# Performance work log

Hardware: AMD Instinct MI355X
Metric: run time of the kernel (lower is better)

Reference implementation:

```python
import jax, jax.numpy as jnp
import numpy as np

N, E = 100000, 800000
D_IN, D_H, D_EMB = 64, 64, 64
L, S = 2, 4
NOISE_SCALE, MIN_U = 0.1, 1e-6


def _xavier(k, shape):
    lim = float(np.sqrt(6.0 / (shape[0] + shape[1])))
    return jax.random.uniform(k, shape, jnp.float32, -lim, lim)


def setup_inputs():
    key = jax.random.key(0)
    ks = jax.random.split(key, 7)
    x = jax.random.normal(ks[0], (N, D_IN), jnp.float32)
    edge_index = jax.random.randint(ks[1], (2, E), 0, N)
    parent_mask = jax.random.bernoulli(ks[2], 0.7, (E,))
    Wi = _xavier(ks[3], (D_IN, D_H))
    bi = jnp.zeros((D_H,), jnp.float32)
    msg_W = jnp.stack([_xavier(jax.random.fold_in(ks[4], l), (2 * D_H, D_H)) for l in range(L)])
    msg_b = jnp.zeros((L, D_H), jnp.float32)
    upd_W = jnp.stack([_xavier(jax.random.fold_in(ks[5], l), (2 * D_H, D_H)) for l in range(L)])
    upd_b = jnp.zeros((L, D_H), jnp.float32)
    Wf = _xavier(ks[6], (D_H, D_EMB))
    bf = jnp.zeros((D_EMB,), jnp.float32)
    return dict(x=x, edge_index=edge_index, parent_mask=parent_mask, Wi=Wi, bi=bi,
                msg_W=msg_W, msg_b=msg_b, upd_W=upd_W, upd_b=upd_b, Wf=Wf, bf=bf)


def _gnn(x, src, dst, mask_f, cnt_inv, Wi, bi, msg_W, msg_b, upd_W, upd_b, Wf, bf):
    # input_proj -> relu, then L rounds of (gather -> message linear -> masked
    # scatter-mean -> update linear -> relu), then final_proj.
    h = jax.nn.relu(x @ Wi + bi)
    for l in range(L):
        Wm, Wu = msg_W[l], upd_W[l]
        # message = Linear(concat(x_i, x_j)); x_i = h[dst] (target), x_j = h[src] (source)
        msg = h[dst] @ Wm[:D_H] + h[src] @ Wm[D_H:] + msg_b[l]  # [E, D_H]
        agg = jax.ops.segment_sum(msg * mask_f[:, None], dst, num_segments=N) * cnt_inv[:, None]
        # update = Linear(concat(x, aggr_out))
        h = jax.nn.relu(h @ Wu[:D_H] + agg @ Wu[D_H:] + upd_b[l])
    return h @ Wf + bf  # [N, D_EMB]


def reference(x, edge_index, parent_mask, Wi, bi, msg_W, msg_b, upd_W, upd_b, Wf, bf):
    src, dst = edge_index[0], edge_index[1]
    mask_f = parent_mask.astype(x.dtype)
    # scatter-mean over causal-parent edges only (0 for nodes without parents, as in PyG)
    cnt = jax.ops.segment_sum(mask_f, dst, num_segments=N)
    cnt_inv = 1.0 / jnp.maximum(cnt, 1.0)
    params = (Wi, bi, msg_W, msg_b, upd_W, upd_b, Wf, bf)
    causal_z = _gnn(x, src, dst, mask_f, cnt_inv, *params)
    # Monte Carlo uncertainty: S perturbed causal embeddings, trace of sample covariance
    noise = jax.random.normal(jax.random.key(42), (S, N, D_IN), x.dtype) * NOISE_SCALE
    zs = jax.lax.map(lambda n: _gnn(x + n, src, dst, mask_f, cnt_inv, *params), noise)  # [S, N, D_EMB]
    mean = zs.mean(axis=0)
    u = jnp.sum((zs - mean[None]) ** 2, axis=(0, 2)) / (S - 1)
    u = jnp.maximum(u, MIN_U)
    return causal_z, u
```

## Files before the change

kernel.cpp:

```cpp
#include <hip/hip_runtime.h>
#include <stdint.h>

#define NN 100000
#define EE 800000
#define GEMM_BX 1563
#define WSTR 72
#define SLAB ((size_t)NN * 64)
#define EDGE_CAP 2304

#define MA_TOTAL 6379
#define MB_TOTAL 7814

typedef unsigned short u16;
typedef __attribute__((ext_vector_type(8))) short bf16x8;
typedef __attribute__((ext_vector_type(4))) float f32x4;

__device__ __forceinline__ uint32_t f2bf(float f) {
  uint32_t u = __float_as_uint(f);
  return (u + 0x7fffu + ((u >> 16) & 1u)) >> 16;
}

__device__ __forceinline__ void tf_round(uint32_t& x0, uint32_t& x1, int r) {
  x0 += x1;
  x1 = (x1 << r) | (x1 >> (32 - r));
  x1 ^= x0;
}

__device__ __forceinline__ void threefry_0_42(uint32_t c0, uint32_t c1,
                                              uint32_t& o0, uint32_t& o1) {
  const uint32_t ks0 = 0u, ks1 = 42u, ks2 = 0x1BD11BDAu ^ 42u;
  uint32_t x0 = c0 + ks0, x1 = c1 + ks1;
  tf_round(x0, x1, 13); tf_round(x0, x1, 15); tf_round(x0, x1, 26); tf_round(x0, x1, 6);
  x0 += ks1; x1 += ks2 + 1u;
  tf_round(x0, x1, 17); tf_round(x0, x1, 29); tf_round(x0, x1, 16); tf_round(x0, x1, 24);
  x0 += ks2; x1 += ks0 + 2u;
  tf_round(x0, x1, 13); tf_round(x0, x1, 15); tf_round(x0, x1, 26); tf_round(x0, x1, 6);
  x0 += ks0; x1 += ks1 + 3u;
  tf_round(x0, x1, 17); tf_round(x0, x1, 29); tf_round(x0, x1, 16); tf_round(x0, x1, 24);
  x0 += ks1; x1 += ks2 + 4u;
  tf_round(x0, x1, 13); tf_round(x0, x1, 15); tf_round(x0, x1, 26); tf_round(x0, x1, 6);
  x0 += ks2; x1 += ks0 + 5u;
  o0 = x0; o1 = x1;
}

__device__ __forceinline__ float noise_val(int s, int n, int d) {
  uint32_t f = (uint32_t)s * 6400000u + (uint32_t)n * 64u + (uint32_t)d;
  uint32_t o0, o1;
  threefry_0_42(0u, f, o0, o1);
  uint32_t bits = o0 ^ o1;
  float v = __uint_as_float((bits >> 9) | 0x3f800000u) - 1.0f;
  const float LO = -0.99999994f;
  float u = v * 2.0f + LO;
  u = fmaxf(u, LO);
  float w = -__logf(fmaf(-u, u, 1.0f));
  float ww = w - 2.5f;
  float p = 2.81022636e-08f;
  p = fmaf(p, ww, 3.43273939e-07f);
  p = fmaf(p, ww, -3.5233877e-06f);
  p = fmaf(p, ww, -4.39150654e-06f);
  p = fmaf(p, ww, 0.00021858087f);
  p = fmaf(p, ww, -0.00125372503f);
  p = fmaf(p, ww, -0.00417768164f);
  p = fmaf(p, ww, 0.246640727f);
  p = fmaf(p, ww, 1.50140941f);
  if (__any(w >= 5.0f)) {
    float ws = sqrtf(w) - 3.0f;
    float p2 = -0.000200214257f;
    p2 = fmaf(p2, ws, 0.000100950558f);
    p2 = fmaf(p2, ws, 0.00134934322f);
    p2 = fmaf(p2, ws, -0.00367342844f);
    p2 = fmaf(p2, ws, 0.00573950773f);
    p2 = fmaf(p2, ws, -0.0076224613f);
    p2 = fmaf(p2, ws, 0.00943887047f);
    p2 = fmaf(p2, ws, 1.00167406f);
    p2 = fmaf(p2, ws, 2.83297682f);
    p = (w < 5.0f) ? p : p2;
  }
  return 0.141421356f * (p * u);
}

__device__ __forceinline__ int mask_at(const void* m, int e, int mode) {
  if (mode == 0) return ((const int*)m)[e] != 0;
  if (mode == 1) return ((const unsigned char*)m)[e] != 0;
  return ((const float*)m)[e] != 0.0f;
}

__global__ void k_pre(const unsigned* mw, int* mode_out,
                      const float* Wi, const float* Wf,
                      const float* msg_b, const float* upd_W,
                      u16* WiT, u16* WfT, float* C1) {
  int b = blockIdx.x, t = threadIdx.x;
  if (b == 0) {
    __shared__ int nonbin, nonfloat;
    if (t == 0) { nonbin = 0; nonfloat = 0; }
    __syncthreads();
    int lb = 0, lf = 0;
    for (int i = t; i < 4096; i += 256) {
      unsigned v = mw[i];
      if (v > 1u) lb = 1;
      if (v != 0u && v != 0x3F800000u) lf = 1;
    }
    if (lb) atomicOr(&nonbin, 1);
    if (lf) atomicOr(&nonfloat, 1);
    __syncthreads();
    if (t == 0)
      mode_out[0] = (nonbin == 0) ? 0 : ((nonfloat == 0) ? 2 : 1);
    return;
  }
  if (b <= 2) {
    const float* W = (b == 1) ? Wi : Wf;
    u16* WT = (b == 1) ? WiT : WfT;
    for (int o = t; o < 4096; o += 256) {
      int k = o >> 6, n = o & 63;
      WT[n * 64 + k] = (u16)f2bf(W[k * 64 + n]);
    }
    return;
  }
  int l = b - 3;
  const float* Wu2 = upd_W + l * 8192 + 4096;
  if (t < 64) {
    float acc = 0.f;
    for (int j = 0; j < 64; ++j) acc = fmaf(msg_b[l * 64 + j], Wu2[j * 64 + t], acc);
    C1[l * 64 + t] = acc;
  }
}

__global__ void k_scan_a(const int* cnt, int* blockSums) {
  __shared__ int sd[256];
  int t = threadIdx.x;
  int base = blockIdx.x * 1024 + t * 4;
  int s = 0;
  #pragma unroll
  for (int j = 0; j < 4; ++j) {
    int i = base + j;
    if (i < NN) s += cnt[i];
  }
  sd[t] = s;
  __syncthreads();
  for (int off = 128; off > 0; off >>= 1) {
    if (t < off) sd[t] += sd[t + off];
    __syncthreads();
  }
  if (t == 0) blockSums[blockIdx.x] = sd[0];
}

__global__ void k_scan_b(int* blockSums, int nb, int* total_out) {
  __shared__ int sd[128];
  int t = threadIdx.x;
  int v = (t < nb) ? blockSums[t] : 0;
  sd[t] = v;
  __syncthreads();
  for (int off = 1; off < 128; off <<= 1) {
    int x = (t >= off) ? sd[t - off] : 0;
    __syncthreads();
    sd[t] += x;
    __syncthreads();
  }
  if (t < nb) blockSums[t] = sd[t] - v;
  if (t == 0) total_out[0] = sd[127];
}

__global__ void k_scan_c(const int* cnt, const int* blockOffs, int* row_ptr,
                         int* cursor, float* cinv) {
  __shared__ int sd[256];
  int t = threadIdx.x;
  int base = blockIdx.x * 1024 + t * 4;
  int v[4], s = 0;
  #pragma unroll
  for (int j = 0; j < 4; ++j) {
    int i = base + j;
    v[j] = (i < NN) ? cnt[i] : 0;
    s += v[j];
  }
  sd[t] = s;
  __syncthreads();
  for (int off = 1; off < 256; off <<= 1) {
    int x = (t >= off) ? sd[t - off] : 0;
    __syncthreads();
    sd[t] += x;
    __syncthreads();
  }
  int excl = sd[t] - s + blockOffs[blockIdx.x];
  #pragma unroll
  for (int j = 0; j < 4; ++j) {
    int i = base + j;
    if (i < NN) {
      row_ptr[i] = excl;
      cursor[i] = excl;
      cinv[i] = 1.0f / fmaxf((float)v[j], 1.0f);
    }
    excl += v[j];
  }
}

__device__ __forceinline__ void mm4(const u16* lW, int m16, int q,
                                    bf16x8 a0, bf16x8 a1, f32x4 (&acc)[4]) {
  #pragma unroll
  for (int nt = 0; nt < 4; ++nt) {
    const u16* wp = lW + (nt * 16 + m16) * WSTR + q * 8;
    bf16x8 b0 = *(const bf16x8*)(wp);
    bf16x8 b1 = *(const bf16x8*)(wp + 32);
    acc[nt] = __builtin_amdgcn_mfma_f32_16x16x32_bf16(a0, b0, acc[nt], 0, 0, 0);
    acc[nt] = __builtin_amdgcn_mfma_f32_16x16x32_bf16(a1, b1, acc[nt], 0, 0, 0);
  }
}

__device__ __forceinline__ void stage_W(const u16* __restrict__ WT, u16* lW) {
  int t = threadIdx.x;
  int r = t >> 2, seg = (t & 3) * 16;
  const uint4* p = (const uint4*)(WT + r * 64 + seg);
  uint4 a = p[0], b = p[1];
  *(uint4*)(lW + r * WSTR + seg) = a;
  *(uint4*)(lW + r * WSTR + seg + 8) = b;
}

__device__ __forceinline__ void stage_H(const u16* __restrict__ Hin, int R0, u16* lT) {
  int t = threadIdx.x;
  int r = t >> 2, seg = (t & 3) * 16;
  int gr = R0 + r;
  uint4 a = {0, 0, 0, 0}, b = {0, 0, 0, 0};
  if (gr < NN) {
    const uint4* p = (const uint4*)(Hin + (size_t)gr * 64 + seg);
    a = p[0]; b = p[1];
  }
  *(uint4*)(lT + r * WSTR + seg) = a;
  *(uint4*)(lT + r * WSTR + seg + 8) = b;
}

__device__ __forceinline__ void input_block(int tile, int inst,
                                            const float* __restrict__ x,
                                            const u16* __restrict__ WiT,
                                            const float* __restrict__ bi,
                                            u16* __restrict__ HoutB,
                                            u16* lW, float* lB) {
  int t = threadIdx.x;
  stage_W(WiT, lW);
  if (t < 64) lB[t] = bi[t];
  int R0 = tile * 64;
  int l = t & 63, w = t >> 6;
  int m16 = l & 15, q = l >> 4;
  int arow = w * 16 + m16;
  int gra = R0 + arow;
  float v[16];
  if (gra < NN) {
    const float4* p0 = (const float4*)(x + (size_t)gra * 64 + q * 8);
    const float4* p1 = (const float4*)(x + (size_t)gra * 64 + q * 8 + 32);
    float4 a = p0[0], b = p0[1], c = p1[0], d = p1[1];
    v[0] = a.x;  v[1] = a.y;  v[2] = a.z;  v[3] = a.w;
    v[4] = b.x;  v[5] = b.y;  v[6] = b.z;  v[7] = b.w;
    v[8] = c.x;  v[9] = c.y;  v[10] = c.z; v[11] = c.w;
    v[12] = d.x; v[13] = d.y; v[14] = d.z; v[15] = d.w;
    if (inst > 0) {
      int s = inst - 1;
      #pragma unroll
      for (int j = 0; j < 8; ++j) v[j] += noise_val(s, gra, q * 8 + j);
      #pragma unroll
      for (int j = 0; j < 8; ++j) v[8 + j] += noise_val(s, gra, q * 8 + 32 + j);
    }
  } else {
    #pragma unroll
    for (int j = 0; j < 16; ++j) v[j] = 0.f;
  }
  union UB { uint32_t u[4]; bf16x8 vv; };
  UB ua, ub;
  #pragma unroll
  for (int jj = 0; jj < 4; ++jj) {
    ua.u[jj] = f2bf(v[2 * jj]) | (f2bf(v[2 * jj + 1]) << 16);
    ub.u[jj] = f2bf(v[8 + 2 * jj]) | (f2bf(v[8 + 2 * jj + 1]) << 16);
  }
  __syncthreads();
  f32x4 acc[4] = {{0.f, 0.f, 0.f, 0.f}, {0.f, 0.f, 0.f, 0.f},
                  {0.f, 0.f, 0.f, 0.f}, {0.f, 0.f, 0.f, 0.f}};
  mm4(lW, m16, q, ua.vv, ub.vv, acc);
  u16* Hout = HoutB + (size_t)inst * SLAB;
  #pragma unroll
  for (int nt = 0; nt < 4; ++nt) {
    int c = nt * 16 + m16;
    #pragma unroll
    for (int r_ = 0; r_ < 4; ++r_) {
      int row = w * 16 + q * 4 + r_;
      int gr = R0 + row;
      if (gr < NN) {
        float z = fmaxf(acc[nt][r_] + lB[c], 0.f);
        Hout[(size_t)gr * 64 + c] = (u16)f2bf(z);
      }
    }
  }
}

__global__ __launch_bounds__(256) void k_megaA(
    const void* __restrict__ mask, const int* __restrict__ dst,
    int* __restrict__ cnt, const int* __restrict__ mode_p,
    const float* __restrict__ x, const u16* __restrict__ WiT,
    const float* __restrict__ bi, u16* __restrict__ HoutB,
    const float* __restrict__ msg_W, const float* __restrict__ upd_W,
    u16* __restrict__ Wu1T, u16* __restrict__ A1T, u16* __restrict__ A2T) {
  __shared__ __align__(16) u16 lW[64 * WSTR];
  __shared__ float lB[64];
  int t = threadIdx.x;
  int bid = blockIdx.x;

  if (bid < 6250) {
    if ((bid & 1) == 0) {
      int e = (bid >> 1) * 256 + t;
      if (e < EE && mask_at(mask, e, *mode_p)) atomicAdd(&cnt[dst[e]], 1);
      return;
    }
    int idx = bid >> 1;
    input_block(idx % GEMM_BX, idx / GEMM_BX, x, WiT, bi, HoutB, lW, lB);
    return;
  }
  if (bid == 6250) {
    input_block(3125 % GEMM_BX, 3125 / GEMM_BX, x, WiT, bi, HoutB, lW, lB);
    return;
  }
  int blk = bid - 6251;
  int l = blk >> 6, b = blk & 63;
  const float* WmT = msg_W + l * 8192;
  const float* WmB = WmT + 4096;
  const float* Wu1 = upd_W + l * 8192;
  const float* Wu2 = Wu1 + 4096;
  float* sd1 = (float*)lW;
  float* sd2 = sd1 + 256;
  int a = t & 63, part = t >> 6;
  float a1 = 0.f, a2 = 0.f;
  #pragma unroll
  for (int jj = 0; jj < 16; ++jj) {
    int j = part * 16 + jj;
    float w2 = Wu2[j * 64 + b];
    a1 = fmaf(WmT[a * 64 + j], w2, a1);
    a2 = fmaf(WmB[a * 64 + j], w2, a2);
  }
  sd1[part * 64 + a] = a1;
  sd2[part * 64 + a] = a2;
  __syncthreads();
  if (t < 64) {
    float s1 = sd1[t] + sd1[64 + t] + sd1[128 + t] + sd1[192 + t];
    float s2 = sd2[t] + sd2[64 + t] + sd2[128 + t] + sd2[192 + t];
    int o = l * 4096 + b * 64 + t;
    A1T[o] = (u16)f2bf(s1);
    A2T[o] = (u16)f2bf(s2);
    Wu1T[o] = (u16)f2bf(Wu1[t * 64 + b]);
  }
}

__global__ __launch_bounds__(256) void k_megaB(
    const void* __restrict__ mask, const int* __restrict__ src,
    const int* __restrict__ dst, int* __restrict__ cursor,
    int* __restrict__ col, const int* __restrict__ mode_p,
    const float* __restrict__ x, const u16* __restrict__ WiT,
    const float* __restrict__ bi, u16* __restrict__ HoutB) {
  __shared__ __align__(16) u16 lW[64 * WSTR];
  __shared__ float lB[64];
  int t = threadIdx.x;
  int bid = blockIdx.x;

  int idx;
  if (bid < 6250) {
    if ((bid & 1) == 0) {
      int e = (bid >> 1) * 256 + t;
      if (e < EE && mask_at(mask, e, *mode_p)) {
        int p = atomicAdd(&cursor[dst[e]], 1);
        col[p] = src[e];
      }
      return;
    }
    idx = bid >> 1;
  } else {
    idx = 3125 + (bid - 6250);
  }
  input_block(idx % GEMM_BX, 2 + idx / GEMM_BX, x, WiT, bi, HoutB, lW, lB);
}

__global__ __launch_bounds__(256) void k_layer(const u16* __restrict__ HinB,
                                               u16* __restrict__ HoutB,
                                               const int* __restrict__ row_ptr,
                                               const int* __restrict__ col,
                                               const float* __restrict__ cinv,
                                               const u16* __restrict__ Wu1T,
                                               const u16* __restrict__ A1T,
                                               const u16* __restrict__ A2T,
                                               const float* __restrict__ b0,
                                               const float* __restrict__ c1) {
  __shared__ __align__(16) u16 lS0[64 * WSTR];
  __shared__ __align__(16) u16 lS1[64 * WSTR];
  __shared__ __align__(16) u16 lW[64 * WSTR];
  __shared__ float lB[128];
  __shared__ float lG[64];
  __shared__ int   lRP[65];
  int* lEdge = (int*)lW;

  int t = threadIdx.x;
  int R0 = blockIdx.x * 64;
  int instBase = blockIdx.y * 2;
  bool two = (instBase + 1) < 5;
  const u16* Hin0 = HinB + (size_t)instBase * SLAB;
  const u16* Hin1 = Hin0 + (two ? SLAB : 0);
  u16* Hout0 = HoutB + (size_t)instBase * SLAB;
  u16* Hout1 = Hout0 + SLAB;

  if (t < 65) {
    int idx = R0 + t;
    if (idx > NN) idx = NN;
    lRP[t] = row_ptr[idx];
  }
  if (t < 64) {
    lB[t] = b0[t];
    lB[64 + t] = c1[t];
  }
  __syncthreads();

  int e0 = lRP[0];
  int nE = lRP[64] - e0;
  bool inLds = (nE <= EDGE_CAP);
  if (inLds) {
    for (int i = t; i < nE; i += 256) lEdge[i] = col[e0 + i];
  }
  if (t < 64) lG[t] = (lRP[t + 1] > lRP[t]) ? 1.f : 0.f;
  __syncthreads();

  {
    int sub = t >> 3, lane8 = t & 7;
    int f0 = lane8 * 8;
    const u16* hb0 = Hin0 + f0;
    const u16* hb1 = Hin1 + f0;
    #pragma unroll
    for (int bb = 0; bb < 2; ++bb) {
      int r = bb * 32 + sub;
      int n = R0 + r;
      float g[8], h[8];
      #pragma unroll
      for (int j = 0; j < 8; ++j) { g[j] = 0.f; h[j] = 0.f; }
      if (n < NN) {
        int e = lRP[r], end = lRP[r + 1];
        int last = end - 1;
        for (; e < end; e += 4) {
          int idx4[4];
          #pragma unroll
          for (int j = 0; j < 4; ++j) {
            int ee = e + j;
            ee = (ee < last) ? ee : last;
            idx4[j] = inLds ? lEdge[ee - e0] : col[ee];
          }
          uint4 P[4];
          #pragma unroll
          for (int j = 0; j < 4; ++j)
            P[j] = *(const uint4*)(hb0 + ((unsigned)idx4[j] << 6));
          uint4 Q[4];
          if (two) {
            #pragma unroll
            for (int j = 0; j < 4; ++j)
              Q[j] = *(const uint4*)(hb1 + ((unsigned)idx4[j] << 6));
          }
          #pragma unroll
          for (int j = 1; j < 4; ++j) {
            bool ok = (e + j) < end;
            P[j].x = ok ? P[j].x : 0u;
            P[j].y = ok ? P[j].y : 0u;
            P[j].z = ok ? P[j].z : 0u;
            P[j].w = ok ? P[j].w : 0u;
            if (two) {
              Q[j].x = ok ? Q[j].x : 0u;
              Q[j].y = ok ? Q[j].y : 0u;
              Q[j].z = ok ? Q[j].z : 0u;
              Q[j].w = ok ? Q[j].w : 0u;
            }
          }
          #pragma unroll
          for (int j = 0; j < 4; ++j) {
            uint4 v = P[j];
            g[0] += __uint_as_float(v.x << 16);
            g[1] += __uint_as_float(v.x & 0xffff0000u);
            g[2] += __uint_as_float(v.y << 16);
            g[3] += __uint_as_float(v.y & 0xffff0000u);
            g[4] += __uint_as_float(v.z << 16);
            g[5] += __uint_as_float(v.z & 0xffff0000u);
            g[6] += __uint_as_float(v.w << 16);
            g[7] += __uint_as_float(v.w & 0xffff0000u);
          }
          if (two) {
            #pragma unroll
            for (int j = 0; j < 4; ++j) {
              uint4 v = Q[j];
              h[0] += __uint_as_float(v.x << 16);
              h[1] += __uint_as_float(v.x & 0xffff0000u);
              h[2] += __uint_as_float(v.y << 16);
              h[3] += __uint_as_float(v.y & 0xffff0000u);
              h[4] += __uint_as_float(v.z << 16);
              h[5] += __uint_as_float(v.z & 0xffff0000u);
              h[6] += __uint_as_float(v.w << 16);
              h[7] += __uint_as_float(v.w & 0xffff0000u);
            }
          }
        }
        float ci = cinv[n];
        #pragma unroll
        for (int j = 0; j < 8; ++j) { g[j] *= ci; h[j] *= ci; }
      }
      uint4 pk;
      pk.x = f2bf(g[0]) | (f2bf(g[1]) << 16);
      pk.y = f2bf(g[2]) | (f2bf(g[3]) << 16);
      pk.z = f2bf(g[4]) | (f2bf(g[5]) << 16);
      pk.w = f2bf(g[6]) | (f2bf(g[7]) << 16);
      *(uint4*)(lS0 + r * WSTR + f0) = pk;
      if (two) {
        uint4 pk2;
        pk2.x = f2bf(h[0]) | (f2bf(h[1]) << 16);
        pk2.y = f2bf(h[2]) | (f2bf(h[3]) << 16);
        pk2.z = f2bf(h[4]) | (f2bf(h[5]) << 16);
        pk2.w = f2bf(h[6]) | (f2bf(h[7]) << 16);
        *(uint4*)(lS1 + r * WSTR + f0) = pk2;
      }
    }
  }
  __syncthreads();

  int l = t & 63, w = t >> 6;
  int m16 = l & 15, q = l >> 4;
  int arow = w * 16 + m16;
  int gra = R0 + arow;
  bf16x8 zz = {0, 0, 0, 0, 0, 0, 0, 0};
  bf16x8 fa0_0 = zz, fa1_0 = zz, fa0_1 = zz, fa1_1 = zz;
  if (gra < NN) {
    const u16* ap = Hin0 + (size_t)gra * 64 + q * 8;
    fa0_0 = *(const bf16x8*)(ap);
    fa1_0 = *(const bf16x8*)(ap + 32);
    if (two) {
      const u16* ap1 = Hin1 + (size_t)gra * 64 + q * 8;
      fa0_1 = *(const bf16x8*)(ap1);
      fa1_1 = *(const bf16x8*)(ap1 + 32);
    }
  }

  stage_W(Wu1T, lW);
  __syncthreads();

  float gA = lG[arow];
  f32x4 acc0[4] = {{0.f, 0.f, 0.f, 0.f}, {0.f, 0.f, 0.f, 0.f},
                   {0.f, 0.f, 0.f, 0.f}, {0.f, 0.f, 0.f, 0.f}};
  f32x4 acc1[4] = {{0.f, 0.f, 0.f, 0.f}, {0.f, 0.f, 0.f, 0.f},
                   {0.f, 0.f, 0.f, 0.f}, {0.f, 0.f, 0.f, 0.f}};
  mm4(lW, m16, q, fa0_0, fa1_0, acc0);
  if (two) mm4(lW, m16, q, fa0_1, fa1_1, acc1);
  __syncthreads();
  stage_W(A1T, lW);
  __syncthreads();
  {
    bf16x8 ga0 = (gA != 0.f) ? fa0_0 : zz;
    bf16x8 ga1 = (gA != 0.f) ? fa1_0 : zz;
    mm4(lW, m16, q, ga0, ga1, acc0);
    if (two) {
      bf16x8 gb0 = (gA != 0.f) ? fa0_1 : zz;
      bf16x8 gb1 = (gA != 0.f) ? fa1_1 : zz;
      mm4(lW, m16, q, gb0, gb1, acc1);
    }
  }
  __syncthreads();
  stage_W(A2T, lW);
  __syncthreads();
  {
    const u16* sRow = lS0 + arow * WSTR + q * 8;
    bf16x8 fs0 = *(const bf16x8*)(sRow);
    bf16x8 fs1 = *(const bf16x8*)(sRow + 32);
    mm4(lW, m16, q, fs0, fs1, acc0);
    if (two) {
      const u16* sRow1 = lS1 + arow * WSTR + q * 8;
      bf16x8 ft0 = *(const bf16x8*)(sRow1);
      bf16x8 ft1 = *(const bf16x8*)(sRow1 + 32);
      mm4(lW, m16, q, ft0, ft1, acc1);
    }
  }
  #pragma unroll
  for (int nt = 0; nt < 4; ++nt) {
    int c = nt * 16 + m16;
    #pragma unroll
    for (int r_ = 0; r_ < 4; ++r_) {
      int row = w * 16 + q * 4 + r_;
      int gr = R0 + row;
      if (gr < NN) {
        float bias = lB[c] + lG[row] * lB[64 + c];
        float v0 = fmaxf(acc0[nt][r_] + bias, 0.f);
        Hout0[(size_t)gr * 64 + c] = (u16)f2bf(v0);
        if (two) {
          float v1 = fmaxf(acc1[nt][r_] + bias, 0.f);
          Hout1[(size_t)gr * 64 + c] = (u16)f2bf(v1);
        }
      }
    }
  }
}

__global__ __launch_bounds__(256) void k_final(const u16* __restrict__ HinB,
                                               const u16* __restrict__ WfT,
                                               const float* __restrict__ bfv,
                                               float* __restrict__ outCausal,
                                               float* __restrict__ out_u) {
  __shared__ __align__(16) u16 lT[64 * WSTR];
  __shared__ __align__(16) u16 lW[64 * WSTR];
  __shared__ float lB[64];
  int t = threadIdx.x;
  int R0 = blockIdx.x * 64;
  stage_W(WfT, lW);
  if (t < 64) lB[t] = bfv[t];
  int l = t & 63, w = t >> 6;
  int m16 = l & 15, q = l >> 4;
  float s1[16], s2[16];
  #pragma unroll
  for (int j = 0; j < 16; ++j) { s1[j] = 0.f; s2[j] = 0.f; }

  for (int inst = 0; inst < 5; ++inst) {
    __syncthreads();
    stage_H(HinB + (size_t)inst * SLAB, R0, lT);
    __syncthreads();
    const u16* aRow = lT + (w * 16 + m16) * WSTR + q * 8;
    bf16x8 fa0 = *(const bf16x8*)(aRow);
    bf16x8 fa1 = *(const bf16x8*)(aRow + 32);
    f32x4 acc[4] = {{0.f, 0.f, 0.f, 0.f}, {0.f, 0.f, 0.f, 0.f},
                    {0.f, 0.f, 0.f, 0.f}, {0.f, 0.f, 0.f, 0.f}};
    mm4(lW, m16, q, fa0, fa1, acc);
    #pragma unroll
    for (int nt = 0; nt < 4; ++nt) {
      int c = nt * 16 + m16;
      #pragma unroll
      for (int r_ = 0; r_ < 4; ++r_) {
        float z = acc[nt][r_] + lB[c];
        if (inst == 0) {
          int gr = R0 + w * 16 + q * 4 + r_;
          if (gr < NN) outCausal[(size_t)gr * 64 + c] = z;
        } else {
          s1[nt * 4 + r_] += z;
          s2[nt * 4 + r_] = fmaf(z, z, s2[nt * 4 + r_]);
        }
      }
    }
  }
  #pragma unroll
  for (int r_ = 0; r_ < 4; ++r_) {
    float pr = 0.f;
    #pragma unroll
    for (int nt = 0; nt < 4; ++nt) {
      float a = s1[nt * 4 + r_];
      pr += s2[nt * 4 + r_] - 0.25f * a * a;
    }
    #pragma unroll
    for (int msk = 1; msk < 16; msk <<= 1)
      pr += __shfl_xor(pr, msk, 64);
    if (m16 == 0) {
      int gr = R0 + w * 16 + q * 4 + r_;
      if (gr < NN) out_u[gr] = fmaxf(pr * (1.0f / 3.0f), 1e-6f);
    }
  }
}

extern "C" void kernel_launch(void* const* d_in, const int* in_sizes, int n_in,
                              void* d_out, int out_size, void* d_ws, size_t ws_size,
                              hipStream_t stream) {
  const float* x      = (const float*)d_in[0];
  const int*   eidx   = (const int*)d_in[1];
  const void*  mask   = d_in[2];
  const float* Wi     = (const float*)d_in[3];
  const float* bi     = (const float*)d_in[4];
  const float* msg_W  = (const float*)d_in[5];
  const float* msg_b  = (const float*)d_in[6];
  const float* upd_W  = (const float*)d_in[7];
  const float* upd_b  = (const float*)d_in[8];
  const float* Wf     = (const float*)d_in[9];
  const float* bfv    = (const float*)d_in[10];

  const int* src = eidx;
  const int* dst = eidx + EE;

  char* ws = (char*)d_ws;
  size_t off = 0;
  auto alloc = [&](size_t bytes) -> void* {
    void* p = ws + off;
    off += (bytes + 255) & ~(size_t)255;
    return p;
  };

  int*   cnt     = (int*)alloc(NN * sizeof(int));
  float* cinv    = (float*)alloc(NN * sizeof(float));
  int*   row_ptr = (int*)alloc((NN + 1) * sizeof(int));
  int*   cursor  = (int*)alloc(NN * sizeof(int));
  int*   col     = (int*)alloc(EE * sizeof(int));
  int*   bsums   = (int*)alloc(128 * sizeof(int));
  int*   mode_p  = (int*)alloc(sizeof(int));
  u16*   Wu1T    = (u16*)alloc(2 * 4096 * sizeof(u16));
  u16*   A1T     = (u16*)alloc(2 * 4096 * sizeof(u16));
  u16*   A2T     = (u16*)alloc(2 * 4096 * sizeof(u16));
  u16*   WiT     = (u16*)alloc(4096 * sizeof(u16));
  u16*   WfT     = (u16*)alloc(4096 * sizeof(u16));
  float* C1      = (float*)alloc(2 * 64 * sizeof(float));
  u16*   HA      = (u16*)alloc(5 * SLAB * sizeof(u16));
  u16*   HB      = (u16*)alloc(5 * SLAB * sizeof(u16));

  float* out_causal = (float*)d_out;
  float* out_u      = (float*)d_out + SLAB;

  k_pre<<<5, 256, 0, stream>>>((const unsigned*)mask, mode_p, Wi, Wf,
                               msg_b, upd_W, WiT, WfT, C1);
  hipMemsetAsync(cnt, 0, NN * sizeof(int), stream);

  k_megaA<<<MA_TOTAL, 256, 0, stream>>>(mask, dst, cnt, mode_p,
                                        x, WiT, bi, HA,
                                        msg_W, upd_W, Wu1T, A1T, A2T);

  const int SCAN_BLKS = (NN + 1023) / 1024;
  k_scan_a<<<SCAN_BLKS, 256, 0, stream>>>(cnt, bsums);
  k_scan_b<<<1, 128, 0, stream>>>(bsums, SCAN_BLKS, row_ptr + NN);
  k_scan_c<<<SCAN_BLKS, 256, 0, stream>>>(cnt, bsums, row_ptr, cursor, cinv);

  k_megaB<<<MB_TOTAL, 256, 0, stream>>>(mask, src, dst, cursor, col, mode_p,
                                        x, WiT, bi, HA);

  dim3 gl(GEMM_BX, 3);
  k_layer<<<gl, 256, 0, stream>>>(HA, HB, row_ptr, col, cinv,
                                  Wu1T, A1T, A2T, upd_b, C1);
  k_layer<<<gl, 256, 0, stream>>>(HB, HA, row_ptr, col, cinv,
                                  Wu1T + 4096, A1T + 4096, A2T + 4096,
                                  upd_b + 64, C1 + 64);
  k_final<<<GEMM_BX, 256, 0, stream>>>(HA, WfT, bfv, out_causal, out_u);

  (void)in_sizes; (void)n_in; (void)out_size; (void)ws_size;
}
```

Baseline: 435.3 us.

## Move all input projections into first mega kernel; split CSR fill; load final A-operand directly

All five input-projection instances now run in the first fused kernel alongside the edge counting and the weight precompute. The CSR column fill becomes its own small kernel after the scan, replacing the second mega kernel. k_final no longer stages H tiles through LDS with two barriers per instance; it loads its bf16 A fragments straight from global memory. This rebalances work across launches and removes LDS traffic and barriers, but it leaves the fill kernel running alone without overlapping GEMM work and uses less coalesced global loads in k_final.

```diff
diff --git a/kernel.cpp b/kernel.cpp
--- a/kernel.cpp
+++ b/kernel.cpp
@@ -8,8 +8,7 @@
 #define SLAB ((size_t)NN * 64)
 #define EDGE_CAP 2304
 
-#define MA_TOTAL 6379
-#define MB_TOTAL 7814
+#define MG_TOTAL 11068
 
 typedef unsigned short u16;
 typedef __attribute__((ext_vector_type(8))) short bf16x8;
@@ -193,6 +192,16 @@
   }
 }
 
+__global__ void k_fill(const void* mask, const int* src, const int* dst,
+                       int* cursor, int* col, const int* mode_p) {
+  int e = blockIdx.x * 256 + threadIdx.x;
+  if (e >= EE) return;
+  if (mask_at(mask, e, *mode_p)) {
+    int p = atomicAdd(&cursor[dst[e]], 1);
+    col[p] = src[e];
+  }
+}
+
 __device__ __forceinline__ void mm4(const u16* lW, int m16, int q,
                                     bf16x8 a0, bf16x8 a1, f32x4 (&acc)[4]) {
   #pragma unroll
@@ -212,19 +221,6 @@
   uint4 a = p[0], b = p[1];
   *(uint4*)(lW + r * WSTR + seg) = a;
   *(uint4*)(lW + r * WSTR + seg + 8) = b;
-}
-
-__device__ __forceinline__ void stage_H(const u16* __restrict__ Hin, int R0, u16* lT) {
-  int t = threadIdx.x;
-  int r = t >> 2, seg = (t & 3) * 16;
-  int gr = R0 + r;
-  uint4 a = {0, 0, 0, 0}, b = {0, 0, 0, 0};
-  if (gr < NN) {
-    const uint4* p = (const uint4*)(Hin + (size_t)gr * 64 + seg);
-    a = p[0]; b = p[1];
-  }
-  *(uint4*)(lT + r * WSTR + seg) = a;
-  *(uint4*)(lT + r * WSTR + seg + 8) = b;
 }
 
 __device__ __forceinline__ void input_block(int tile, int inst,
@@ -288,7 +284,7 @@
   }
 }
 
-__global__ __launch_bounds__(256) void k_megaA(
+__global__ __launch_bounds__(256) void k_mega(
     const void* __restrict__ mask, const int* __restrict__ dst,
     int* __restrict__ cnt, const int* __restrict__ mode_p,
     const float* __restrict__ x, const u16* __restrict__ WiT,
@@ -300,21 +296,22 @@
   int t = threadIdx.x;
   int bid = blockIdx.x;
 
+  int idx = -1;
   if (bid < 6250) {
     if ((bid & 1) == 0) {
       int e = (bid >> 1) * 256 + t;
       if (e < EE && mask_at(mask, e, *mode_p)) atomicAdd(&cnt[dst[e]], 1);
       return;
     }
-    int idx = bid >> 1;
+    idx = bid >> 1;
+  } else if (bid < 10940) {
+    idx = 3125 + (bid - 6250);
+  }
+  if (idx >= 0) {
     input_block(idx % GEMM_BX, idx / GEMM_BX, x, WiT, bi, HoutB, lW, lB);
     return;
   }
-  if (bid == 6250) {
-    input_block(3125 % GEMM_BX, 3125 / GEMM_BX, x, WiT, bi, HoutB, lW, lB);
-    return;
-  }
-  int blk = bid - 6251;
+  int blk = bid - 10940;
   int l = blk >> 6, b = blk & 63;
   const float* WmT = msg_W + l * 8192;
   const float* WmB = WmT + 4096;
@@ -342,34 +339,6 @@
     A2T[o] = (u16)f2bf(s2);
     Wu1T[o] = (u16)f2bf(Wu1[t * 64 + b]);
   }
-}
-
-__global__ __launch_bounds__(256) void k_megaB(
-    const void* __restrict__ mask, const int* __restrict__ src,
-    const int* __restrict__ dst, int* __restrict__ cursor,
-    int* __restrict__ col, const int* __restrict__ mode_p,
-    const float* __restrict__ x, const u16* __restrict__ WiT,
-    const float* __restrict__ bi, u16* __restrict__ HoutB) {
-  __shared__ __align__(16) u16 lW[64 * WSTR];
-  __shared__ float lB[64];
-  int t = threadIdx.x;
-  int bid = blockIdx.x;
-
-  int idx;
-  if (bid < 6250) {
-    if ((bid & 1) == 0) {
-      int e = (bid >> 1) * 256 + t;
-      if (e < EE && mask_at(mask, e, *mode_p)) {
-        int p = atomicAdd(&cursor[dst[e]], 1);
-        col[p] = src[e];
-      }
-      return;
-    }
-    idx = bid >> 1;
-  } else {
-    idx = 3125 + (bid - 6250);
-  }
-  input_block(idx % GEMM_BX, 2 + idx / GEMM_BX, x, WiT, bi, HoutB, lW, lB);
 }
 
 __global__ __launch_bounds__(256) void k_layer(const u16* __restrict__ HinB,
@@ -595,7 +564,6 @@
                                                const float* __restrict__ bfv,
                                                float* __restrict__ outCausal,
                                                float* __restrict__ out_u) {
-  __shared__ __align__(16) u16 lT[64 * WSTR];
   __shared__ __align__(16) u16 lW[64 * WSTR];
   __shared__ float lB[64];
   int t = threadIdx.x;
@@ -604,17 +572,21 @@
   if (t < 64) lB[t] = bfv[t];
   int l = t & 63, w = t >> 6;
   int m16 = l & 15, q = l >> 4;
+  int arow = w * 16 + m16;
+  int gra = R0 + arow;
+  bf16x8 zz = {0, 0, 0, 0, 0, 0, 0, 0};
   float s1[16], s2[16];
   #pragma unroll
   for (int j = 0; j < 16; ++j) { s1[j] = 0.f; s2[j] = 0.f; }
+  __syncthreads();
 
   for (int inst = 0; inst < 5; ++inst) {
-    __syncthreads();
-    stage_H(HinB + (size_t)inst * SLAB, R0, lT);
-    __syncthreads();
-    const u16* aRow = lT + (w * 16 + m16) * WSTR + q * 8;
-    bf16x8 fa0 = *(const bf16x8*)(aRow);
-    bf16x8 fa1 = *(const bf16x8*)(aRow + 32);
+    bf16x8 fa0 = zz, fa1 = zz;
+    if (gra < NN) {
+      const u16* ap = HinB + (size_t)inst * SLAB + (size_t)gra * 64 + q * 8;
+      fa0 = *(const bf16x8*)(ap);
+      fa1 = *(const bf16x8*)(ap + 32);
+    }
     f32x4 acc[4] = {{0.f, 0.f, 0.f, 0.f}, {0.f, 0.f, 0.f, 0.f},
                     {0.f, 0.f, 0.f, 0.f}, {0.f, 0.f, 0.f, 0.f}};
     mm4(lW, m16, q, fa0, fa1, acc);
@@ -701,17 +673,15 @@
                                msg_b, upd_W, WiT, WfT, C1);
   hipMemsetAsync(cnt, 0, NN * sizeof(int), stream);
 
-  k_megaA<<<MA_TOTAL, 256, 0, stream>>>(mask, dst, cnt, mode_p,
-                                        x, WiT, bi, HA,
-                                        msg_W, upd_W, Wu1T, A1T, A2T);
+  k_mega<<<MG_TOTAL, 256, 0, stream>>>(mask, dst, cnt, mode_p,
+                                       x, WiT, bi, HA,
+                                       msg_W, upd_W, Wu1T, A1T, A2T);
 
   const int SCAN_BLKS = (NN + 1023) / 1024;
   k_scan_a<<<SCAN_BLKS, 256, 0, stream>>>(cnt, bsums);
   k_scan_b<<<1, 128, 0, stream>>>(bsums, SCAN_BLKS, row_ptr + NN);
   k_scan_c<<<SCAN_BLKS, 256, 0, stream>>>(cnt, bsums, row_ptr, cursor, cinv);
-
-  k_megaB<<<MB_TOTAL, 256, 0, stream>>>(mask, src, dst, cursor, col, mode_p,
-                                        x, WiT, bi, HA);
+  k_fill<<<EE / 256, 256, 0, stream>>>(mask, src, dst, cursor, col, mode_p);
 
   dim3 gl(GEMM_BX, 3);
   k_layer<<<gl, 256, 0, stream>>>(HA, HB, row_ptr, col, cinv,
```

Result: no change. 427.7 us (-1.7%).
